# Optimization experiments

Hardware: AMD Instinct MI355X
Metric: run time of the kernel (lower is better)

Reference implementation:

```python
import jax, jax.numpy as jnp
import numpy as np

BS, L, H, HD, R, HID = 4, 2048, 12, 64, 16, 768


def setup_inputs() -> dict:
    key = jax.random.key(0)
    k0, k1, k2, k3 = jax.random.split(key, 4)
    xavier = np.sqrt(2.0 / (H + HD))  # xavier_normal_ on (H, HD)
    lin = 1.0 / np.sqrt(HID)
    return {
        "hidden_states": jax.random.normal(k0, (BS, L, HID), jnp.float32),
        "K1_w": jax.random.normal(k1, (HID, H * HD), jnp.float32) * lin,
        "K1_b": jnp.zeros((H * HD,), jnp.float32),
        "V1_w": jax.random.normal(k2, (HID, H * HD), jnp.float32) * lin,
        "V1_b": jnp.zeros((H * HD,), jnp.float32),
        "ReadingHead": jax.random.normal(k3, (H, HD), jnp.float32) * xavier,
        "bidirection_weight": jnp.full((1, 1, H, 1, 2 * R), 1.0 / (2 * R), jnp.float32),
    }


def _scan_mmap(valid_mask, reverse):
    # valid_mask: (bs, L, H) bool. Sequential register-shift scan over positions 1..L-1.
    bs, Ln, Hn = valid_mask.shape
    idxs = jnp.arange(1, Ln, dtype=jnp.int32)
    masks = jnp.swapaxes(valid_mask[:, 1:], 0, 1)  # (L-1, bs, H)
    if reverse:
        idxs = idxs[::-1]
        masks = masks[::-1]
    init = jnp.zeros((bs, R + 1, Hn), jnp.int32)

    def step(valids, xm):
        i, m = xm
        valids = valids.at[:, 0].set(i)  # slot 0 <- current index (matches in-place torch order)
        shifted = jnp.where(m[:, None, :], valids[:, :-1], valids[:, 1:])
        valids = valids.at[:, 1:].set(shifted)
        return valids, valids[:, 1:]

    _, out = jax.lax.scan(step, init, (idxs, masks))  # (L-1, bs, R, H)
    if reverse:
        out = out[::-1]
    out = jnp.concatenate([jnp.zeros((1, bs, R, Hn), jnp.int32), out], axis=0)
    return jnp.swapaxes(out, 0, 1)  # (bs, L, R, H)


def reference(hidden_states, K1_w, K1_b, V1_w, V1_b, ReadingHead, bidirection_weight):
    K1 = jax.nn.relu(hidden_states @ K1_w + K1_b).reshape(BS, L, H, HD)
    V1 = jax.nn.relu(hidden_states @ V1_w + V1_b).reshape(BS, L, H, HD)
    dot_products = jnp.einsum('blhn,hn->blh', K1, ReadingHead)
    valid_mask = dot_products > 0.5  # attn_var default branch
    fm = _scan_mmap(valid_mask, False).reshape(BS, L * R, H)
    bm = _scan_mmap(valid_mask, True).reshape(BS, L * R, H)
    V_forward = jnp.take_along_axis(V1, fm[..., None], axis=1).reshape(BS, L, R, H, HD)
    V_backward = jnp.take_along_axis(V1, bm[..., None], axis=1).reshape(BS, L, R, H, HD)
    w = bidirection_weight[0, 0, :, 0, :]  # (H, 2R); first R -> forward, last R -> backward
    ctx = (jnp.einsum('blrhd,hr->blhd', V_forward, w[:, :R])
           + jnp.einsum('blrhd,hr->blhd', V_backward, w[:, R:]))
    return ctx.reshape(BS, L, H * HD)
```

## Files before the change

### kernel.cpp

```cpp
#include <hip/hip_runtime.h>
#include <hip/hip_bf16.h>

#define BS 4
#define L 2048
#define H 12
#define HD 64
#define R 16
#define HID 768
#define MARGIN 0.02f
#define FIXCAP 16384
#define FIXGRID 1024

typedef __attribute__((ext_vector_type(8))) short s8v;
typedef __attribute__((ext_vector_type(4))) float f32x4;

static __device__ __forceinline__ unsigned short f2bf_bits(float f) {
    __hip_bfloat16 h = __float2bfloat16(f);
    return *reinterpret_cast<unsigned short*>(&h);
}

__global__ void zero_cnt(int* __restrict__ cnt) { if (threadIdx.x == 0) *cnt = 0; }

__global__ __launch_bounds__(256) void convert_hs(
    const float* __restrict__ in, __hip_bfloat16* __restrict__ out)
{
    int i = (blockIdx.x * 256 + threadIdx.x) * 4;
    float4 v = *(const float4*)&in[i];
    ushort4 o;
    o.x = f2bf_bits(v.x); o.y = f2bf_bits(v.y);
    o.z = f2bf_bits(v.z); o.w = f2bf_bits(v.w);
    *(ushort4*)&out[i] = o;
}

__global__ __launch_bounds__(256) void transpose_wt(
    const float* __restrict__ in, __hip_bfloat16* __restrict__ out)
{
    __shared__ float s[32][33];
    const int c = threadIdx.x & 31, r8 = threadIdx.x >> 5;
    const int kt = blockIdx.x * 32, nt = blockIdx.y * 32;
#pragma unroll
    for (int rr = 0; rr < 4; ++rr) {
        int k = r8 + rr * 8;
        s[k][c] = in[(size_t)(kt + k) * HID + nt + c];
    }
    __syncthreads();
#pragma unroll
    for (int rr = 0; rr < 4; ++rr) {
        int n = r8 + rr * 8;
        out[(size_t)(nt + n) * HID + kt + c] = __float2bfloat16(s[c][n]);
    }
}

__global__ __launch_bounds__(256) void gemm_fused(
    const __hip_bfloat16* __restrict__ A,
    const __hip_bfloat16* __restrict__ WtK,
    const __hip_bfloat16* __restrict__ WtV,
    const float* __restrict__ K1b,
    const float* __restrict__ V1b,
    const float* __restrict__ RH,
    float* __restrict__ dots,
    int* __restrict__ fixlist,
    int* __restrict__ fixcnt,
    __hip_bfloat16* __restrict__ C)
{
    __shared__ __hip_bfloat16 As[128][40];
    __shared__ __hip_bfloat16 Bs[128][40];

    const int tid = threadIdx.x;
    const bool isV = blockIdx.y < 6;
    const int m0 = blockIdx.x * 128;
    const int n0 = (isV ? blockIdx.y : blockIdx.y - 6) * 128;
    const __hip_bfloat16* Bt = isV ? WtV : WtK;

    const int wid = tid >> 6, lane = tid & 63;
    const int quad = lane >> 4, lm = lane & 15;
    const int wm = wid & 1, wn = wid >> 1;

    f32x4 acc[4][4] = {};

    for (int k0 = 0; k0 < HID; k0 += 32) {
#pragma unroll
        for (int it = 0; it < 2; ++it) {
            int slot = tid + it * 256;
            int r = slot >> 2, kq = slot & 3;
            *(float4*)&As[r][kq * 8] =
                *(const float4*)&A[(size_t)(m0 + r) * HID + k0 + kq * 8];
        }
#pragma unroll
        for (int it = 0; it < 2; ++it) {
            int slot = tid + it * 256;
            int r = slot >> 2, kq = slot & 3;
            *(float4*)&Bs[r][kq * 8] =
                *(const float4*)&Bt[(size_t)(n0 + r) * HID + k0 + kq * 8];
        }
        __syncthreads();
        s8v af[4], bf[4];
#pragma unroll
        for (int i = 0; i < 4; ++i)
            af[i] = *(const s8v*)&As[wm * 64 + i * 16 + lm][quad * 8];
#pragma unroll
        for (int j = 0; j < 4; ++j)
            bf[j] = *(const s8v*)&Bs[wn * 64 + j * 16 + lm][quad * 8];
#pragma unroll
        for (int i = 0; i < 4; ++i)
#pragma unroll
            for (int j = 0; j < 4; ++j)
                acc[i][j] = __builtin_amdgcn_mfma_f32_16x16x32_bf16(
                    af[i], bf[j], acc[i][j], 0, 0, 0);
        __syncthreads();
    }

    if (isV) {
#pragma unroll
        for (int i = 0; i < 4; ++i) {
            int row_b = m0 + wm * 64 + i * 16 + quad * 4;
#pragma unroll
            for (int j = 0; j < 4; ++j) {
                int col = n0 + wn * 64 + j * 16 + lm;
                float bsv = V1b[col];
#pragma unroll
                for (int reg = 0; reg < 4; ++reg) {
                    float v = acc[i][j][reg] + bsv;
                    C[(size_t)(row_b + reg) * HID + col] =
                        __float2bfloat16(fmaxf(v, 0.f));
                }
            }
        }
    } else {
        const int head = (n0 >> 6) + wn;
        float bj[4], rj[4];
#pragma unroll
        for (int j = 0; j < 4; ++j) {
            bj[j] = K1b[head * 64 + j * 16 + lm];
            rj[j] = RH[head * 64 + j * 16 + lm];
        }
#pragma unroll
        for (int i = 0; i < 4; ++i) {
            int row0 = m0 + wm * 64 + i * 16 + quad * 4;
#pragma unroll
            for (int reg = 0; reg < 4; ++reg) {
                float p = 0.f;
#pragma unroll
                for (int j = 0; j < 4; ++j)
                    p = fmaf(fmaxf(acc[i][j][reg] + bj[j], 0.f), rj[j], p);
                p += __shfl_xor(p, 1, 64);
                p += __shfl_xor(p, 2, 64);
                p += __shfl_xor(p, 4, 64);
                p += __shfl_xor(p, 8, 64);
                if (lm == 0) {
                    int row = row0 + reg;
                    int b = row >> 11, l = row & (L - 1);
                    dots[((b * H + head) << 11) + l] = p;
                    if (fabsf(p - 0.5f) < MARGIN) {
                        int idx = atomicAdd(fixcnt, 1);
                        if (idx < FIXCAP) fixlist[idx] = row * 16 + head;
                    }
                }
            }
        }
    }
}

__global__ __launch_bounds__(256) void fixup_kernel(
    const float* __restrict__ hs,
    const float* __restrict__ W,
    const float* __restrict__ bias,
    const float* __restrict__ RH,
    const int* __restrict__ fixlist,
    const int* __restrict__ fixcnt,
    float* __restrict__ dots)
{
    __shared__ float hrow[HID];
    __shared__ float psum[4][64];

    const int tid = threadIdx.x;
    const int n = min(*fixcnt, FIXCAP);

    for (int item = blockIdx.x; item < n; item += FIXGRID) {
        int packed = fixlist[item];
        int row = packed >> 4, head = packed & 15;
        int b = row >> 11, l = row & (L - 1);

#pragma unroll
        for (int i = 0; i < 3; ++i)
            hrow[tid + i * 256] = hs[(size_t)row * HID + tid + i * 256];
        __syncthreads();

        const int d = tid & 63, kq = tid >> 6;
        float a0 = 0.f, a1 = 0.f;
#pragma unroll 8
        for (int i = 0; i < 96; ++i) {
            int k = kq + i * 8;
            a0 = fmaf(W[(size_t)k * HID + head * 64 + d], hrow[k], a0);
            a1 = fmaf(W[(size_t)(k + 4) * HID + head * 64 + d], hrow[k + 4], a1);
        }
        psum[kq][d] = a0 + a1;
        __syncthreads();
        if (tid < 64) {
            float v = psum[0][tid] + psum[1][tid] + psum[2][tid] +
                      psum[3][tid] + bias[head * 64 + tid];
            v = fmaxf(v, 0.f) * RH[head * 64 + tid];
#pragma unroll
            for (int s = 1; s < 64; s <<= 1) v += __shfl_xor(v, s, 64);
            if (tid == 0) dots[((size_t)(b * H + head) << 11) + l] = v;
        }
        __syncthreads();
    }
}

__global__ __launch_bounds__(256) void scan_kernel(
    const float* __restrict__ dots,
    short* __restrict__ fm,
    short* __restrict__ bm)
{
    __shared__ unsigned short P[L];
    __shared__ unsigned short S[L];
    __shared__ int wsum[4];

    const int bh = blockIdx.x;
    const int b = bh / H, h = bh % H;
    const int tid = threadIdx.x;
    const int base = tid * 8;
    const int lane = tid & 63, w = tid >> 6;

    int m[8], c[8];
    int run = 0;
#pragma unroll
    for (int i = 0; i < 8; ++i) {
        int l = base + i;
        m[i] = (l >= 1 && dots[((size_t)bh << 11) + l] > 0.5f) ? 1 : 0;
        run += m[i];
        c[i] = run;
    }
    int sc = run;
#pragma unroll
    for (int s = 1; s < 64; s <<= 1) {
        int v = __shfl_up(sc, s, 64);
        if (lane >= s) sc += v;
    }
    if (lane == 63) wsum[w] = sc;
    __syncthreads();
    int woff = 0;
    for (int i = 0; i < 4; ++i) if (i < w) woff += wsum[i];
    const int ex = woff + sc - run;

#pragma unroll
    for (int i = 0; i < 8; ++i) {
        int l = base + i;
        int pc = ex + c[i];
        P[l] = (unsigned short)pc;
        if (m[i]) S[pc] = (unsigned short)l;
    }
    __syncthreads();
    const int T = P[L - 1];

#pragma unroll
    for (int i = 0; i < 8; ++i) {
        int l = base + i;
        int cc = ex + c[i];
        union { unsigned short s[16]; uint4 q[2]; } uf, ub;
#pragma unroll
        for (int r = 0; r < 16; ++r)
            uf.s[r] = (cc - r >= 1) ? S[cc - r] : (unsigned short)0;
        int cp = (l >= 1) ? (int)P[l - 1] : 0;
#pragma unroll
        for (int r = 0; r < 16; ++r) {
            int j = cp + 1 + r;
            ub.s[r] = (l >= 1 && j <= T) ? S[j] : (unsigned short)0;
        }
        size_t off = ((size_t)(b * L + l) * H + h) * R;
        *(uint4*)&fm[off] = uf.q[0];
        *(uint4*)&fm[off + 8] = uf.q[1];
        *(uint4*)&bm[off] = ub.q[0];
        *(uint4*)&bm[off + 8] = ub.q[1];
    }
}

__global__ __launch_bounds__(192) void gather_kernel(
    const __hip_bfloat16* __restrict__ V1,
    const short* __restrict__ fm,
    const short* __restrict__ bm,
    const float* __restrict__ bw,
    float* __restrict__ out)
{
    __shared__ short sidx[2][2][H][R];
    __shared__ float sw[2][H][R];

    const int bl0 = blockIdx.x * 2;
    const int b = bl0 >> 11;
    const int tid = threadIdx.x;

    for (int i = tid; i < 2 * 2 * H * R; i += 192) {
        int ls = i / (2 * H * R), rem = i % (2 * H * R);
        int dir = rem / (H * R), hr = rem % (H * R);
        int h = hr >> 4, r = hr & 15;
        const short* src = dir ? bm : fm;
        sidx[ls][dir][h][r] = src[((size_t)(bl0 + ls) * H + h) * R + r];
    }
    for (int i = tid; i < 2 * H * R; i += 192) {
        int dir = i / (H * R), hr = i % (H * R);
        int h = hr >> 4, r = hr & 15;
        sw[dir][h][r] = bw[h * (2 * R) + dir * R + r];
    }
    __syncthreads();

    const int ls = tid / 96, t = tid % 96;
    const int h = t >> 3, d8 = t & 7;
    const __hip_bfloat16* Vb = V1 + (size_t)b * L * HID;

    float a[8] = {};
#pragma unroll
    for (int slot = 0; slot < 32; ++slot) {
        int dir = slot >> 4, r = slot & 15;
        int idx = sidx[ls][dir][h][r];
        float wv = sw[dir][h][r];
        const __hip_bfloat16* p = Vb + (size_t)idx * HID + h * HD + d8 * 8;
        uint4 uv = *(const uint4*)p;
        a[0] = fmaf(wv, __uint_as_float(uv.x << 16), a[0]);
        a[1] = fmaf(wv, __uint_as_float(uv.x & 0xffff0000u), a[1]);
        a[2] = fmaf(wv, __uint_as_float(uv.y << 16), a[2]);
        a[3] = fmaf(wv, __uint_as_float(uv.y & 0xffff0000u), a[3]);
        a[4] = fmaf(wv, __uint_as_float(uv.z << 16), a[4]);
        a[5] = fmaf(wv, __uint_as_float(uv.z & 0xffff0000u), a[5]);
        a[6] = fmaf(wv, __uint_as_float(uv.w << 16), a[6]);
        a[7] = fmaf(wv, __uint_as_float(uv.w & 0xffff0000u), a[7]);
    }
    float* op = &out[(size_t)(bl0 + ls) * HID + h * HD + d8 * 8];
    float4 o0, o1;
    o0.x = a[0]; o0.y = a[1]; o0.z = a[2]; o0.w = a[3];
    o1.x = a[4]; o1.y = a[5]; o1.z = a[6]; o1.w = a[7];
    *(float4*)op = o0;
    *(float4*)(op + 4) = o1;
}

extern "C" void kernel_launch(void* const* d_in, const int* in_sizes, int n_in,
                              void* d_out, int out_size, void* d_ws, size_t ws_size,
                              hipStream_t stream) {
    const float* hs  = (const float*)d_in[0];
    const float* K1w = (const float*)d_in[1];
    const float* K1b = (const float*)d_in[2];
    const float* V1w = (const float*)d_in[3];
    const float* V1b = (const float*)d_in[4];
    const float* RH  = (const float*)d_in[5];
    const float* bw  = (const float*)d_in[6];
    float* out = (float*)d_out;

    __hip_bfloat16* Abf = (__hip_bfloat16*)d_out;

    char* ws = (char*)d_ws;
    __hip_bfloat16* WtV = (__hip_bfloat16*)ws;
    __hip_bfloat16* WtK = (__hip_bfloat16*)(ws + 1179648);
    __hip_bfloat16* V1  = (__hip_bfloat16*)(ws + 2359296);
    float* dots = (float*)(ws + 14942208);
    short* fm   = (short*)(ws + 15335424);
    short* bm   = (short*)(ws + 18481152);
    int* fixlist = (int*)(ws + 21626880);
    int* fixcnt  = (int*)(ws + 21692416);

    convert_hs<<<(BS * L * HID) / (256 * 4), 256, 0, stream>>>(hs, Abf);
    transpose_wt<<<dim3(HID / 32, HID / 32), 256, 0, stream>>>(V1w, WtV);
    transpose_wt<<<dim3(HID / 32, HID / 32), 256, 0, stream>>>(K1w, WtK);
    zero_cnt<<<1, 64, 0, stream>>>(fixcnt);
    gemm_fused<<<dim3(BS * L / 128, 12), 256, 0, stream>>>(
        Abf, WtK, WtV, K1b, V1b, RH, dots, fixlist, fixcnt, V1);
    fixup_kernel<<<FIXGRID, 256, 0, stream>>>(hs, K1w, K1b, RH, fixlist, fixcnt, dots);
    scan_kernel<<<BS * H, 256, 0, stream>>>(dots, fm, bm);
    gather_kernel<<<BS * L / 2, 192, 0, stream>>>(V1, fm, bm, bw, out);
}
```

Measured before the change: 187.9 us.

## Load GEMM tiles via direct global-to-LDS with XOR swizzle and merge setup kernels

The GEMM now stages A and B tiles with global_load_lds, writing straight into unpadded LDS under an XOR swizzle. This skips the register round-trip and the bank conflicts the padding used to avoid. Separately, the two weight-transpose launches are merged into one 3D grid, and the counter zeroing is folded into convert_hs, which removes two kernel launches. The swizzle mapping must match exactly between the load and fragment-read sides, or the MFMA inputs will be wrong.

```diff
diff --git a/kernel.cpp b/kernel.cpp
--- a/kernel.cpp
+++ b/kernel.cpp
@@ -14,16 +14,21 @@
 typedef __attribute__((ext_vector_type(8))) short s8v;
 typedef __attribute__((ext_vector_type(4))) float f32x4;
 
+typedef __attribute__((address_space(1))) const void as1_void;
+typedef __attribute__((address_space(3))) void as3_void;
+#define GLOAD_LDS16(g, l) \
+    __builtin_amdgcn_global_load_lds((as1_void*)(g), (as3_void*)(l), 16, 0, 0)
+
 static __device__ __forceinline__ unsigned short f2bf_bits(float f) {
     __hip_bfloat16 h = __float2bfloat16(f);
     return *reinterpret_cast<unsigned short*>(&h);
 }
 
-__global__ void zero_cnt(int* __restrict__ cnt) { if (threadIdx.x == 0) *cnt = 0; }
-
 __global__ __launch_bounds__(256) void convert_hs(
-    const float* __restrict__ in, __hip_bfloat16* __restrict__ out)
-{
+    const float* __restrict__ in, __hip_bfloat16* __restrict__ out,
+    int* __restrict__ fixcnt)
+{
+    if (blockIdx.x == 0 && threadIdx.x == 0) *fixcnt = 0;
     int i = (blockIdx.x * 256 + threadIdx.x) * 4;
     float4 v = *(const float4*)&in[i];
     ushort4 o;
@@ -32,9 +37,12 @@
     *(ushort4*)&out[i] = o;
 }
 
-__global__ __launch_bounds__(256) void transpose_wt(
-    const float* __restrict__ in, __hip_bfloat16* __restrict__ out)
-{
+__global__ __launch_bounds__(256) void transpose_wt2(
+    const float* __restrict__ K1w, const float* __restrict__ V1w,
+    __hip_bfloat16* __restrict__ WtK, __hip_bfloat16* __restrict__ WtV)
+{
+    const float* in = blockIdx.z ? V1w : K1w;
+    __hip_bfloat16* out = blockIdx.z ? WtV : WtK;
     __shared__ float s[32][33];
     const int c = threadIdx.x & 31, r8 = threadIdx.x >> 5;
     const int kt = blockIdx.x * 32, nt = blockIdx.y * 32;
@@ -63,8 +71,8 @@
     int* __restrict__ fixcnt,
     __hip_bfloat16* __restrict__ C)
 {
-    __shared__ __hip_bfloat16 As[128][40];
-    __shared__ __hip_bfloat16 Bs[128][40];
+    __shared__ alignas(16) __hip_bfloat16 As[128 * 32];
+    __shared__ alignas(16) __hip_bfloat16 Bs[128 * 32];
 
     const int tid = threadIdx.x;
     const bool isV = blockIdx.y < 6;
@@ -76,31 +84,40 @@
     const int quad = lane >> 4, lm = lane & 15;
     const int wm = wid & 1, wn = wid >> 1;
 
+    const int rsub = lane >> 2;
+    const int csw  = (lane & 3) ^ ((lane >> 3) & 3);
+    const __hip_bfloat16* gA0 =
+        A + (size_t)(m0 + 32 * wid + rsub) * HID + csw * 8;
+    const __hip_bfloat16* gA1 = gA0 + (size_t)16 * HID;
+    const __hip_bfloat16* gB0 =
+        Bt + (size_t)(n0 + 32 * wid + rsub) * HID + csw * 8;
+    const __hip_bfloat16* gB1 = gB0 + (size_t)16 * HID;
+    __hip_bfloat16* lA0 = &As[(32 * wid) * 32];
+    __hip_bfloat16* lA1 = &As[(32 * wid + 16) * 32];
+    __hip_bfloat16* lB0 = &Bs[(32 * wid) * 32];
+    __hip_bfloat16* lB1 = &Bs[(32 * wid + 16) * 32];
+
+    const int fsw = (lm >> 1) & 3;
+    const __hip_bfloat16* pA = &As[(wm * 64 + lm) * 32 + ((quad ^ fsw) * 8)];
+    const __hip_bfloat16* pB = &Bs[(wn * 64 + lm) * 32 + ((quad ^ fsw) * 8)];
+
     f32x4 acc[4][4] = {};
 
     for (int k0 = 0; k0 < HID; k0 += 32) {
-#pragma unroll
-        for (int it = 0; it < 2; ++it) {
-            int slot = tid + it * 256;
-            int r = slot >> 2, kq = slot & 3;
-            *(float4*)&As[r][kq * 8] =
-                *(const float4*)&A[(size_t)(m0 + r) * HID + k0 + kq * 8];
-        }
-#pragma unroll
-        for (int it = 0; it < 2; ++it) {
-            int slot = tid + it * 256;
-            int r = slot >> 2, kq = slot & 3;
-            *(float4*)&Bs[r][kq * 8] =
-                *(const float4*)&Bt[(size_t)(n0 + r) * HID + k0 + kq * 8];
-        }
-        __syncthreads();
+        GLOAD_LDS16(gA0, lA0);
+        GLOAD_LDS16(gA1, lA1);
+        GLOAD_LDS16(gB0, lB0);
+        GLOAD_LDS16(gB1, lB1);
+        gA0 += 32; gA1 += 32; gB0 += 32; gB1 += 32;
+        __syncthreads();
+
         s8v af[4], bf[4];
 #pragma unroll
         for (int i = 0; i < 4; ++i)
-            af[i] = *(const s8v*)&As[wm * 64 + i * 16 + lm][quad * 8];
+            af[i] = *(const s8v*)(pA + i * 16 * 32);
 #pragma unroll
         for (int j = 0; j < 4; ++j)
-            bf[j] = *(const s8v*)&Bs[wn * 64 + j * 16 + lm][quad * 8];
+            bf[j] = *(const s8v*)(pB + j * 16 * 32);
 #pragma unroll
         for (int i = 0; i < 4; ++i)
 #pragma unroll
@@ -357,10 +374,8 @@
     int* fixlist = (int*)(ws + 21626880);
     int* fixcnt  = (int*)(ws + 21692416);
 
-    convert_hs<<<(BS * L * HID) / (256 * 4), 256, 0, stream>>>(hs, Abf);
-    transpose_wt<<<dim3(HID / 32, HID / 32), 256, 0, stream>>>(V1w, WtV);
-    transpose_wt<<<dim3(HID / 32, HID / 32), 256, 0, stream>>>(K1w, WtK);
-    zero_cnt<<<1, 64, 0, stream>>>(fixcnt);
+    convert_hs<<<(BS * L * HID) / (256 * 4), 256, 0, stream>>>(hs, Abf, fixcnt);
+    transpose_wt2<<<dim3(HID / 32, HID / 32, 2), 256, 0, stream>>>(K1w, V1w, WtK, WtV);
     gemm_fused<<<dim3(BS * L / 128, 12), 256, 0, stream>>>(
         Abf, WtK, WtV, K1b, V1b, RH, dots, fixlist, fixcnt, V1);
     fixup_kernel<<<FIXGRID, 256, 0, stream>>>(hs, K1w, K1b, RH, fixlist, fixcnt, dots);
```

Result: faster. 180.7 us (-3.8%).
